# Kernel optimization log

Hardware: AMD Instinct MI355X
Metric: run time of the kernel (lower is better)

The kernel has to match this reference:

```python
import jax, jax.numpy as jnp
import numpy as np

N_BLOCK = 3; EMBED = 256; N_HEAD = 8; HEAD = EMBED // N_HEAD
N_AGENT = 8; SEQ = 256; BATCH = 64; ACT_DIM = 32
DECAY_SCALE = 1.0
EPS = 1e-6


def _decay_matrix():
    # Per-head decay kappas as in Mava Sable, decay over timesteps (pos // n_agent), causal mask.
    gammas = (1.0 - jnp.exp(jnp.linspace(jnp.log(1.0 / 32.0), jnp.log(1.0 / 512.0), N_HEAD))) * DECAY_SCALE
    t = (jnp.arange(SEQ) // N_AGENT).astype(jnp.float32)
    diff = t[:, None] - t[None, :]
    causal = jnp.arange(SEQ)[:, None] >= jnp.arange(SEQ)[None, :]
    return jnp.where(causal[None], gammas[:, None, None] ** diff[None], 0.0)  # [H,S,S]


def rmsnorm(x, scale):
    return x * jax.lax.rsqrt(jnp.mean(x * x, -1, keepdims=True) + EPS) * scale


def groupnorm(x, scale, bias):
    # GroupNorm with n_head groups over the feature dim, per position.
    B, S, E = x.shape
    xg = x.reshape(B, S, N_HEAD, HEAD)
    mu = xg.mean(-1, keepdims=True)
    var = ((xg - mu) ** 2).mean(-1, keepdims=True)
    xn = ((xg - mu) * jax.lax.rsqrt(var + 1e-5)).reshape(B, S, E)
    return xn * scale + bias


def retention(q_in, k_in, v_in, wq, wk, wv, wg, wo, gns, gnb, decay):
    # Parallel multi-scale retention: (Q K^T * D) V, groupnorm, swish gate from query input.
    B, S, E = q_in.shape
    q = (q_in @ wq).reshape(B, S, N_HEAD, HEAD).transpose(0, 2, 1, 3)
    k = (k_in @ wk).reshape(B, S, N_HEAD, HEAD).transpose(0, 2, 1, 3) / jnp.sqrt(jnp.float32(HEAD))
    v = (v_in @ wv).reshape(B, S, N_HEAD, HEAD).transpose(0, 2, 1, 3)
    scores = jnp.einsum('bhnd,bhmd->bhnm', q, k) * decay[None]
    ret = jnp.einsum('bhnm,bhmd->bhnd', scores, v)
    ret = groupnorm(ret.transpose(0, 2, 1, 3).reshape(B, S, E), gns, gnb)
    return (jax.nn.swish(q_in @ wg) * ret) @ wo


def swiglu(x, wg, w1, w2):
    return (jax.nn.swish(x @ wg) * (x @ w1)) @ w2


def forward(action, obs_rep, w_enc, ln0, wq1, wk1, wv1, wg1, wo1, gns1, gnb1, ln1,
            wq2, wk2, wv2, wg2, wo2, gns2, gnb2, ln2, swg, sw1, sw2, ln3,
            hw1, hb1, hln, hw2, hb2):
    decay = _decay_matrix()
    x = rmsnorm(jax.nn.gelu(action @ w_enc), ln0)
    for b in range(N_BLOCK):
        r1 = retention(x, x, x, wq1[b], wk1[b], wv1[b], wg1[b], wo1[b], gns1[b], gnb1[b], decay)
        x = rmsnorm(x + r1, ln1[b])
        r2 = retention(obs_rep, x, x, wq2[b], wk2[b], wv2[b], wg2[b], wo2[b], gns2[b], gnb2[b], decay)
        x = rmsnorm(obs_rep + r2, ln2[b])
        x = rmsnorm(x + swiglu(x, swg[b], sw1[b], sw2[b]), ln3[b])
    h = rmsnorm(jax.nn.gelu(x @ hw1 + hb1), hln)
    return h @ hw2 + hb2


def setup_inputs() -> dict:
    key = jax.random.key(0)
    ks = jax.random.split(key, 24)
    E, A, NB = EMBED, ACT_DIM, N_BLOCK
    s = 0.02
    return {
        'action': jax.random.uniform(ks[0], (BATCH, SEQ, A), jnp.float32),
        'obs_rep': jax.random.normal(ks[1], (BATCH, SEQ, E), jnp.float32),
        'w_enc': jax.random.normal(ks[2], (A, E), jnp.float32) * s,
        'ln0': jnp.ones((E,), jnp.float32),
        'wq1': jax.random.normal(ks[3], (NB, E, E), jnp.float32) * s,
        'wk1': jax.random.normal(ks[4], (NB, E, E), jnp.float32) * s,
        'wv1': jax.random.normal(ks[5], (NB, E, E), jnp.float32) * s,
        'wg1': jax.random.normal(ks[6], (NB, E, E), jnp.float32) * s,
        'wo1': jax.random.normal(ks[7], (NB, E, E), jnp.float32) * s,
        'gns1': jnp.ones((NB, E), jnp.float32),
        'gnb1': jnp.zeros((NB, E), jnp.float32),
        'ln1': jnp.ones((NB, E), jnp.float32),
        'wq2': jax.random.normal(ks[8], (NB, E, E), jnp.float32) * s,
        'wk2': jax.random.normal(ks[9], (NB, E, E), jnp.float32) * s,
        'wv2': jax.random.normal(ks[10], (NB, E, E), jnp.float32) * s,
        'wg2': jax.random.normal(ks[11], (NB, E, E), jnp.float32) * s,
        'wo2': jax.random.normal(ks[12], (NB, E, E), jnp.float32) * s,
        'gns2': jnp.ones((NB, E), jnp.float32),
        'gnb2': jnp.zeros((NB, E), jnp.float32),
        'ln2': jnp.ones((NB, E), jnp.float32),
        'swg': jax.random.normal(ks[13], (NB, E, E), jnp.float32) * s,
        'sw1': jax.random.normal(ks[14], (NB, E, E), jnp.float32) * s,
        'sw2': jax.random.normal(ks[15], (NB, E, E), jnp.float32) * s,
        'ln3': jnp.ones((NB, E), jnp.float32),
        'hw1': jax.random.normal(ks[16], (E, E), jnp.float32) * s,
        'hb1': jnp.zeros((E,), jnp.float32),
        'hln': jnp.ones((E,), jnp.float32),
        'hw2': jax.random.normal(ks[17], (E, A), jnp.float32) * s,
        'hb2': jnp.zeros((A,), jnp.float32),
    }


def reference(action, obs_rep, w_enc, ln0, wq1, wk1, wv1, wg1, wo1, gns1, gnb1, ln1,
              wq2, wk2, wv2, wg2, wo2, gns2, gnb2, ln2, swg, sw1, sw2, ln3,
              hw1, hb1, hln, hw2, hb2):
    return forward(action, obs_rep, w_enc, ln0, wq1, wk1, wv1, wg1, wo1, gns1, gnb1, ln1,
                   wq2, wk2, wv2, wg2, wo2, gns2, gnb2, ln2, swg, sw1, sw2, ln3,
                   hw1, hb1, hln, hw2, hb2)
```

## Files before the change

kernel.cpp:

```cpp
#include <hip/hip_runtime.h>
#include <cstdint>
#include <cmath>

typedef __attribute__((ext_vector_type(8))) short short8;
typedef __attribute__((ext_vector_type(4))) float floatx4;

#define DEV static __device__ __forceinline__

DEV float bf2f(uint16_t u) {
    union { uint32_t i; float f; } v; v.i = ((uint32_t)u) << 16; return v.f;
}
DEV uint16_t f2bf(float f) {
    union { float f; uint32_t i; } v; v.f = f;
    uint32_t r = (v.i + 0x7FFFu + ((v.i >> 16) & 1u)) >> 16;
    return (uint16_t)r;
}
DEV float swishf(float x) { return x / (1.f + __expf(-x)); }
DEV float geluf(float x) {
    const float c = 0.7978845608028654f;
    float t = tanhf(c * (x + 0.044715f * x * x * x));
    return 0.5f * x * (1.f + t);
}

#define CHUNK_E 8192
#define MAT_E   65536
#define APAD    264


struct TArg { const float* src[15]; };

__global__ __launch_bounds__(256) void tpose_k(TArg ta, uint16_t* __restrict__ arena) {
    int z = blockIdx.z;
    const float* src; uint16_t* dst;
    if (z == 0) {
        if (blockIdx.y) return;
        src = ta.src[0]; dst = arena;
    } else if (z <= 39) {
        int q = z - 1; int ti = q / 3, s = q % 3;
        src = ta.src[1 + ti] + (size_t)s * 65536;
        dst = arena + CHUNK_E + (size_t)(ti * 3 + s) * MAT_E;
    } else {
        src = ta.src[14]; dst = arena + CHUNK_E + (size_t)39 * MAT_E;
    }
    int k0 = blockIdx.y << 5;
    int n0 = blockIdx.x << 6;
    __shared__ __align__(16) uint16_t tile[32][72];
    int t = threadIdx.x;
    {
        int r = t >> 3, c = (t & 7) << 3;
        const float* s0 = src + (size_t)(k0 + r) * 256 + n0 + c;
        float4 f0 = *(const float4*)s0;
        float4 f1 = *(const float4*)(s0 + 4);
        tile[r][c + 0] = f2bf(f0.x); tile[r][c + 1] = f2bf(f0.y);
        tile[r][c + 2] = f2bf(f0.z); tile[r][c + 3] = f2bf(f0.w);
        tile[r][c + 4] = f2bf(f1.x); tile[r][c + 5] = f2bf(f1.y);
        tile[r][c + 6] = f2bf(f1.z); tile[r][c + 7] = f2bf(f1.w);
    }
    __syncthreads();
    {
        int n = t >> 2, c = (t & 3) << 3;
        uint16_t tmp[8];
#pragma unroll
        for (int j = 0; j < 8; ++j) tmp[j] = tile[c + j][n];
        *(uint4*)&dst[(size_t)(k0 >> 5) * CHUNK_E + (size_t)(n0 + n) * 32 + c] = *(uint4*)tmp;
    }
}

struct SegArgs {
    const float* action; const float* obs;
    uint16_t *actb, *obsb, *xb, *bq, *bk, *bv, *bg, *brg;
    const float *ln0, *hb1, *hln, *hw2, *hb2;
    float* outp;
    float l2g[8];
};

enum { EP_NONE = 0, EP_GELU_RMS = 1, EP_RESID_RMS = 2 };
enum { EP2_NONE = 0, EP2_SWIGLU = 1 };

template<int EPI, int K, int LDA, bool OG, int LDO, bool RL>
DEV void gemm_u(int m0,
                const uint16_t* __restrict__ A,
                const uint16_t* __restrict__ Wt,
                uint16_t* __restrict__ Og,
                uint16_t* __restrict__ Ol,
                const float* __restrict__ bias,
                const uint16_t* __restrict__ Rg,
                const uint16_t* __restrict__ Rl,
                const float* __restrict__ lnw,
                float (&rowsum)[8][32])
{
    const int t = threadIdx.x;
    const int w = t >> 6, lane = t & 63, l16 = lane & 15, lg = lane >> 4;
    constexpr int NC = K / 32;

    floatx4 acc[2][2];
#pragma unroll
    for (int i = 0; i < 2; ++i)
#pragma unroll
        for (int j = 0; j < 2; ++j) acc[i][j] = (floatx4){0.f, 0.f, 0.f, 0.f};

#pragma unroll
    for (int kc = 0; kc < NC; ++kc) {
        short8 aF[2], bF[2];
#pragma unroll
        for (int rt = 0; rt < 2; ++rt) {
            int row = (rt << 4) + l16;
            if constexpr (LDA != 0)
                aF[rt] = *(const short8*)(A + (size_t)row * LDA + (kc << 5) + (lg << 3));
            else
                aF[rt] = *(const short8*)(A + (size_t)(m0 + row) * K + (kc << 5) + (lg << 3));
        }
#pragma unroll
        for (int ct = 0; ct < 2; ++ct)
            bF[ct] = *(const short8*)(Wt + (size_t)kc * CHUNK_E +
                                      (size_t)((w << 5) + (ct << 4) + l16) * 32 + (lg << 3));
#pragma unroll
        for (int rt = 0; rt < 2; ++rt)
#pragma unroll
            for (int ct = 0; ct < 2; ++ct)
                acc[rt][ct] = __builtin_amdgcn_mfma_f32_16x16x32_bf16(
                    aF[rt], bF[ct], acc[rt][ct], 0, 0, 0);
    }

    float v[2][2][4];
#pragma unroll
    for (int rt = 0; rt < 2; ++rt)
#pragma unroll
        for (int ct = 0; ct < 2; ++ct)
#pragma unroll
            for (int r = 0; r < 4; ++r) {
                int row = (rt << 4) + (lg << 2) + r;
                int col = (w << 5) + (ct << 4) + l16;
                float x = acc[rt][ct][r];
                if constexpr (EPI == EP_GELU_RMS) {
                    if (bias) x += bias[col];
                    x = geluf(x);
                }
                if constexpr (EPI == EP_RESID_RMS) {
                    if constexpr (RL) x += bf2f(Rl[(size_t)row * APAD + col]);
                    else              x += bf2f(Rg[(size_t)(m0 + row) * 256 + col]);
                }
                v[rt][ct][r] = x;
            }

    if constexpr (EPI == EP_GELU_RMS || EPI == EP_RESID_RMS) {
#pragma unroll
        for (int rt = 0; rt < 2; ++rt)
#pragma unroll
            for (int r = 0; r < 4; ++r) {
                float p = v[rt][0][r] * v[rt][0][r] + v[rt][1][r] * v[rt][1][r];
                p += __shfl_xor(p, 1, 64); p += __shfl_xor(p, 2, 64);
                p += __shfl_xor(p, 4, 64); p += __shfl_xor(p, 8, 64);
                int row = (rt << 4) + (lg << 2) + r;
                if (l16 == 0) rowsum[w][row] = p;
            }
        __syncthreads();
#pragma unroll
        for (int rt = 0; rt < 2; ++rt)
#pragma unroll
            for (int r = 0; r < 4; ++r) {
                int row = (rt << 4) + (lg << 2) + r;
                float tot = rowsum[0][row] + rowsum[1][row] + rowsum[2][row] + rowsum[3][row]
                          + rowsum[4][row] + rowsum[5][row] + rowsum[6][row] + rowsum[7][row];
                float rn = rsqrtf(tot * (1.f / 256.f) + 1e-6f);
#pragma unroll
                for (int ct = 0; ct < 2; ++ct) {
                    int col = (w << 5) + (ct << 4) + l16;
                    uint16_t bb = f2bf(v[rt][ct][r] * rn * lnw[col]);
                    if constexpr (OG)
                        Og[(size_t)(m0 + row) * 256 + col] = bb;
                    if constexpr (LDO != 0)
                        Ol[(size_t)row * LDO + col] = bb;
                }
            }
        __syncthreads();
    } else {
#pragma unroll
        for (int rt = 0; rt < 2; ++rt)
#pragma unroll
            for (int ct = 0; ct < 2; ++ct)
#pragma unroll
                for (int r = 0; r < 4; ++r) {
                    int row = (rt << 4) + (lg << 2) + r;
                    int col = (w << 5) + (ct << 4) + l16;
                    uint16_t bb = f2bf(v[rt][ct][r]);
                    if constexpr (OG)
                        Og[(size_t)(m0 + row) * 256 + col] = bb;
                    if constexpr (LDO != 0)
                        Ol[(size_t)row * LDO + col] = bb;
                }
    }
}

template<int EPI, int LDA>
DEV void gemm2_u(int m0, const uint16_t* __restrict__ A,
                 const uint16_t* __restrict__ W1, const uint16_t* __restrict__ W2,
                 uint16_t* __restrict__ O1, uint16_t* __restrict__ O2,
                 uint16_t* __restrict__ Ol)
{
    const int t = threadIdx.x;
    const int w = t >> 6, lane = t & 63, l16 = lane & 15, lg = lane >> 4;

    floatx4 a1[2][2], a2[2][2];
#pragma unroll
    for (int i = 0; i < 2; ++i)
#pragma unroll
        for (int j = 0; j < 2; ++j) {
            a1[i][j] = (floatx4){0.f, 0.f, 0.f, 0.f};
            a2[i][j] = (floatx4){0.f, 0.f, 0.f, 0.f};
        }

#pragma unroll
    for (int kc = 0; kc < 8; ++kc) {
        short8 aF[2], b1[2], b2[2];
#pragma unroll
        for (int rt = 0; rt < 2; ++rt) {
            int row = (rt << 4) + l16;
            if constexpr (LDA != 0)
                aF[rt] = *(const short8*)(A + (size_t)row * LDA + (kc << 5) + (lg << 3));
            else
                aF[rt] = *(const short8*)(A + (size_t)(m0 + row) * 256 + (kc << 5) + (lg << 3));
        }
        size_t woff = (size_t)kc * CHUNK_E + (size_t)((w << 5) + l16) * 32 + (lg << 3);
#pragma unroll
        for (int ct = 0; ct < 2; ++ct) {
            b1[ct] = *(const short8*)(W1 + woff + (size_t)(ct << 4) * 32);
            b2[ct] = *(const short8*)(W2 + woff + (size_t)(ct << 4) * 32);
        }
#pragma unroll
        for (int rt = 0; rt < 2; ++rt)
#pragma unroll
            for (int ct = 0; ct < 2; ++ct) {
                a1[rt][ct] = __builtin_amdgcn_mfma_f32_16x16x32_bf16(aF[rt], b1[ct], a1[rt][ct], 0, 0, 0);
                a2[rt][ct] = __builtin_amdgcn_mfma_f32_16x16x32_bf16(aF[rt], b2[ct], a2[rt][ct], 0, 0, 0);
            }
    }

#pragma unroll
    for (int rt = 0; rt < 2; ++rt)
#pragma unroll
        for (int ct = 0; ct < 2; ++ct)
#pragma unroll
            for (int r = 0; r < 4; ++r) {
                int row = (rt << 4) + (lg << 2) + r;
                int col = (w << 5) + (ct << 4) + l16;
                if constexpr (EPI == EP2_NONE) {
                    size_t idx = (size_t)(m0 + row) * 256 + col;
                    O1[idx] = f2bf(a1[rt][ct][r]);
                    O2[idx] = f2bf(a2[rt][ct][r]);
                } else {
                    Ol[(size_t)row * APAD + col] = f2bf(swishf(a1[rt][ct][r]) * a2[rt][ct][r]);
                }
            }
}

DEV int rowbase(int blk) { return (blk & 63) * 256 + (blk >> 6) * 32; }


__global__ __launch_bounds__(512, 4) void seg0_k(SegArgs sa, const uint16_t* __restrict__ wenc,
                                                 const uint16_t* __restrict__ wq,
                                                 const uint16_t* __restrict__ wk,
                                                 const uint16_t* __restrict__ wv,
                                                 const uint16_t* __restrict__ wg)
{
    __shared__ float rowsum[8][32];
    __shared__ __align__(16) uint16_t actS[32][40];
    __shared__ __align__(16) uint16_t T0[32][APAD];
    const int t = threadIdx.x;
    const int m0 = rowbase(blockIdx.x);
    if (t < 256) {
        int r = t >> 3, c = (t & 7) << 2;
        float4 f = *(const float4*)(sa.action + (size_t)(m0 + r) * 32 + c);
        uint16_t tmp[4] = { f2bf(f.x), f2bf(f.y), f2bf(f.z), f2bf(f.w) };
        *(uint2*)&actS[r][c] = *(uint2*)tmp;
    }
    {
        const float4* ob = (const float4*)sa.obs + (size_t)m0 * 64;
        uint2* od = (uint2*)sa.obsb + (size_t)m0 * 64;
#pragma unroll
        for (int j = 0; j < 4; ++j) {
            float4 f = ob[(j << 9) + t];
            uint16_t tmp[4] = { f2bf(f.x), f2bf(f.y), f2bf(f.z), f2bf(f.w) };
            od[(j << 9) + t] = *(uint2*)tmp;
        }
    }
    __syncthreads();
    gemm_u<EP_GELU_RMS, 32, 40, true, APAD, false>(m0, &actS[0][0], wenc,
        sa.xb, &T0[0][0], nullptr, nullptr, nullptr, sa.ln0, rowsum);
    gemm2_u<EP2_NONE, APAD>(m0, &T0[0][0], wq, wk, sa.bq, sa.bk, nullptr);
    gemm2_u<EP2_NONE, APAD>(m0, &T0[0][0], wv, wg, sa.bv, sa.bg, nullptr);
}

__global__ __launch_bounds__(512, 4) void attn_k(SegArgs sa, const float* __restrict__ gns,
                                                 const float* __restrict__ gnb)
{
    __shared__ __align__(16) uint16_t QS[256][40];
    __shared__ __align__(16) uint16_t Ks[256][40];
    __shared__ __align__(16) uint16_t Vt[32][264];
    const int b = blockIdx.x & 63, h = blockIdx.x >> 6;
    const float l2g = sa.l2g[h];
    const int t = threadIdx.x, w = t >> 6, lane = t & 63, l16 = lane & 15, lg = lane >> 4;
    const size_t base = ((size_t)b * 256) * 256 + (size_t)h * 32;
    const uint16_t *q = sa.bq, *kbuf = sa.bk, *vbuf = sa.bv, *g = sa.bg;
    uint16_t* out = sa.brg;

    if (t < 256) {
        const uint4* qr = (const uint4*)(q + base + (size_t)t * 256);
        *(uint4*)&QS[t][0] = qr[0]; *(uint4*)&QS[t][8] = qr[1];
        *(uint4*)&QS[t][16] = qr[2]; *(uint4*)&QS[t][24] = qr[3];
        const uint4* kr = (const uint4*)(kbuf + base + (size_t)t * 256);
        *(uint4*)&Ks[t][0] = kr[0]; *(uint4*)&Ks[t][8] = kr[1];
        *(uint4*)&Ks[t][16] = kr[2]; *(uint4*)&Ks[t][24] = kr[3];
    } else {
        int c = t - 256;
        union { uint4 v4[4]; uint16_t u[32]; } vv;
        const uint4* vr = (const uint4*)(vbuf + base + (size_t)c * 256);
        vv.v4[0] = vr[0]; vv.v4[1] = vr[1]; vv.v4[2] = vr[2]; vv.v4[3] = vr[3];
#pragma unroll
        for (int d = 0; d < 32; ++d) Vt[d][c] = vv.u[d];
    }
    __syncthreads();

    short8 qF[2];
#pragma unroll
    for (int rt = 0; rt < 2; ++rt)
        qF[rt] = *(const short8*)&QS[(w << 5) + (rt << 4) + l16][lg << 3];

    floatx4 racc[2][2];
#pragma unroll
    for (int i = 0; i < 2; ++i) { racc[i][0] = (floatx4){0,0,0,0}; racc[i][1] = (floatx4){0,0,0,0}; }

    const float invsq = 0.17677669529663687f;
    const int jtmax = w;
    for (int jt = 0; jt <= jtmax; ++jt) {
        const int j0 = jt << 5;
        floatx4 sacc[2][2];
#pragma unroll
        for (int i = 0; i < 2; ++i) { sacc[i][0] = (floatx4){0,0,0,0}; sacc[i][1] = (floatx4){0,0,0,0}; }
        short8 kF[2];
#pragma unroll
        for (int ct = 0; ct < 2; ++ct)
            kF[ct] = *(const short8*)&Ks[j0 + (ct << 4) + l16][lg << 3];
#pragma unroll
        for (int rt = 0; rt < 2; ++rt)
#pragma unroll
            for (int ct = 0; ct < 2; ++ct)
                sacc[rt][ct] = __builtin_amdgcn_mfma_f32_16x16x32_bf16(
                    qF[rt], kF[ct], sacc[rt][ct], 0, 0, 0);
#pragma unroll
        for (int rt = 0; rt < 2; ++rt)
#pragma unroll
            for (int ct = 0; ct < 2; ++ct)
#pragma unroll
                for (int r = 0; r < 4; ++r) {
                    int row = (rt << 4) + (lg << 2) + r;
                    int i = (w << 5) + row;
                    int j = j0 + (ct << 4) + l16;
                    float svv = 0.f;
                    if (i >= j)
                        svv = sacc[rt][ct][r] * invsq *
                              exp2f((float)((i >> 3) - (j >> 3)) * l2g);
                    QS[(w << 5) + row][(ct << 4) + l16] = f2bf(svv);
                }
        short8 vF[2];
#pragma unroll
        for (int ct = 0; ct < 2; ++ct)
            vF[ct] = *(const short8*)&Vt[(ct << 4) + l16][j0 + (lg << 3)];
#pragma unroll
        for (int rt = 0; rt < 2; ++rt) {
            short8 sF = *(const short8*)&QS[(w << 5) + (rt << 4) + l16][lg << 3];
#pragma unroll
            for (int ct = 0; ct < 2; ++ct)
                racc[rt][ct] = __builtin_amdgcn_mfma_f32_16x16x32_bf16(
                    sF, vF[ct], racc[rt][ct], 0, 0, 0);
        }
    }

#pragma unroll
    for (int rt = 0; rt < 2; ++rt)
#pragma unroll
        for (int r = 0; r < 4; ++r) {
            float v0 = racc[rt][0][r], v1 = racc[rt][1][r];
            float s1 = v0 + v1, s2 = v0 * v0 + v1 * v1;
            s1 += __shfl_xor(s1, 1, 64); s2 += __shfl_xor(s2, 1, 64);
            s1 += __shfl_xor(s1, 2, 64); s2 += __shfl_xor(s2, 2, 64);
            s1 += __shfl_xor(s1, 4, 64); s2 += __shfl_xor(s2, 4, 64);
            s1 += __shfl_xor(s1, 8, 64); s2 += __shfl_xor(s2, 8, 64);
            float mu = s1 * (1.f / 32.f);
            float var = s2 * (1.f / 32.f) - mu * mu;
            float rstd = rsqrtf(var + 1e-5f);
            int srow = (w << 5) + (rt << 4) + (lg << 2) + r;
            size_t obase = ((size_t)b * 256 + srow) * 256 + (size_t)h * 32;
#pragma unroll
            for (int ct = 0; ct < 2; ++ct) {
                int d = (ct << 4) + l16;
                float x = ct ? v1 : v0;
                float y = (x - mu) * rstd * gns[h * 32 + d] + gnb[h * 32 + d];
                float gv = swishf(bf2f(g[obase + d]));
                out[obase + d] = f2bf(y * gv);
            }
        }
}

__global__ __launch_bounds__(512, 4) void g1_k(SegArgs sa,
    const uint16_t* __restrict__ wo, const float* __restrict__ ln1,
    const uint16_t* __restrict__ wq, const uint16_t* __restrict__ wk,
    const uint16_t* __restrict__ wv, const uint16_t* __restrict__ wg)
{
    __shared__ float rowsum[8][32];
    __shared__ __align__(16) uint16_t T0[32][APAD];
    const int m0 = rowbase(blockIdx.x);
    gemm_u<EP_RESID_RMS, 256, 0, false, APAD, false>(m0, sa.brg, wo,
        nullptr, &T0[0][0], nullptr, sa.xb, nullptr, ln1, rowsum);
    gemm2_u<EP2_NONE, APAD>(m0, &T0[0][0], wk, wv, sa.bk, sa.bv, nullptr);
    gemm2_u<EP2_NONE, 0>(m0, sa.obsb, wq, wg, sa.bq, sa.bg, nullptr);
}

__global__ __launch_bounds__(512, 4) void g2_k(SegArgs sa,
    const uint16_t* __restrict__ wo, const float* __restrict__ ln2,
    const uint16_t* __restrict__ wswg, const uint16_t* __restrict__ wsw1,
    const uint16_t* __restrict__ wsw2, const float* __restrict__ ln3,
    const uint16_t* __restrict__ nwq, const uint16_t* __restrict__ nwk,
    const uint16_t* __restrict__ nwv, const uint16_t* __restrict__ nwg)
{
    __shared__ float rowsum[8][32];
    __shared__ __align__(16) uint16_t T0[32][APAD];
    __shared__ __align__(16) uint16_t T1[32][APAD];
    const int m0 = rowbase(blockIdx.x);
    gemm_u<EP_RESID_RMS, 256, 0, false, APAD, false>(m0, sa.brg, wo,
        nullptr, &T0[0][0], nullptr, sa.obsb, nullptr, ln2, rowsum);
    gemm2_u<EP2_SWIGLU, APAD>(m0, &T0[0][0], wswg, wsw1, nullptr, nullptr, &T1[0][0]);
    __syncthreads();
    gemm_u<EP_RESID_RMS, 256, APAD, true, APAD, true>(m0, &T1[0][0], wsw2,
        sa.xb, &T0[0][0], nullptr, nullptr, &T0[0][0], ln3, rowsum);
    if (nwq) {
        gemm2_u<EP2_NONE, APAD>(m0, &T0[0][0], nwq, nwk, sa.bq, sa.bk, nullptr);
        gemm2_u<EP2_NONE, APAD>(m0, &T0[0][0], nwv, nwg, sa.bv, sa.bg, nullptr);
    }
}

__global__ __launch_bounds__(512, 4) void head_k(SegArgs sa, const uint16_t* __restrict__ hw1t)
{
    __shared__ float rowsum[8][32];
    __shared__ float w2s[8192];
    __shared__ __align__(16) uint16_t T0[32][APAD];
    const int t = threadIdx.x;
    const int m0 = rowbase(blockIdx.x);
#pragma unroll
    for (int j = 0; j < 16; ++j) w2s[(j << 9) + t] = sa.hw2[(j << 9) + t];
    gemm_u<EP_GELU_RMS, 256, 0, false, APAD, false>(m0, sa.xb, hw1t,
        nullptr, &T0[0][0], sa.hb1, nullptr, nullptr, sa.hln, rowsum);
    {
        int n = t & 31, rs = t >> 5;
#pragma unroll
        for (int rr = 0; rr < 2; ++rr) {
            int lrow = (rr << 4) + rs;
            float a0 = sa.hb2[n];
#pragma unroll 8
            for (int kk = 0; kk < 256; ++kk)
                a0 += bf2f(T0[lrow][kk]) * w2s[kk * 32 + n];
            sa.outp[(size_t)(m0 + lrow) * 32 + n] = a0;
        }
    }
}

extern "C" void kernel_launch(void* const* d_in, const int* in_sizes, int n_in,
                              void* d_out, int out_size, void* d_ws, size_t ws_size,
                              hipStream_t stream)
{
    const float* action = (const float*)d_in[0];
    const float* obs    = (const float*)d_in[1];
    const float* w_enc  = (const float*)d_in[2];
    const float* ln0    = (const float*)d_in[3];
    const float* wq1 = (const float*)d_in[4];
    const float* wk1 = (const float*)d_in[5];
    const float* wv1 = (const float*)d_in[6];
    const float* wg1 = (const float*)d_in[7];
    const float* wo1 = (const float*)d_in[8];
    const float* gns1 = (const float*)d_in[9];
    const float* gnb1 = (const float*)d_in[10];
    const float* ln1  = (const float*)d_in[11];
    const float* wq2 = (const float*)d_in[12];
    const float* wk2 = (const float*)d_in[13];
    const float* wv2 = (const float*)d_in[14];
    const float* wg2 = (const float*)d_in[15];
    const float* wo2 = (const float*)d_in[16];
    const float* gns2 = (const float*)d_in[17];
    const float* gnb2 = (const float*)d_in[18];
    const float* ln2  = (const float*)d_in[19];
    const float* swgp = (const float*)d_in[20];
    const float* sw1p = (const float*)d_in[21];
    const float* sw2p = (const float*)d_in[22];
    const float* ln3  = (const float*)d_in[23];
    const float* hw1  = (const float*)d_in[24];
    const float* hb1  = (const float*)d_in[25];
    const float* hln  = (const float*)d_in[26];
    const float* hw2  = (const float*)d_in[27];
    const float* hb2  = (const float*)d_in[28];

    char* ws = (char*)d_ws;
    uint16_t* wt   = (uint16_t*)(ws + 0);
    uint16_t* actb = (uint16_t*)(ws + 6291456);
    uint16_t* obsb = (uint16_t*)(ws + 7340032);
    uint16_t* xb   = (uint16_t*)(ws + 15728640);
    uint16_t* bq   = (uint16_t*)(ws + 24117248);
    uint16_t* bk   = (uint16_t*)(ws + 32505856);
    uint16_t* bv   = (uint16_t*)(ws + 40894464);
    uint16_t* bg   = (uint16_t*)(ws + 49283072);
    uint16_t* brg  = (uint16_t*)(ws + 57671680);

    uint16_t* wtenc = wt;
    uint16_t* hw1t  = wt + CHUNK_E + (size_t)39 * MAT_E;
    auto WTp = [&](int ti, int s) { return wt + CHUNK_E + (size_t)(ti * 3 + s) * MAT_E; };

    TArg ta;
    ta.src[0] = w_enc;
    ta.src[1] = wq1;  ta.src[2] = wk1;  ta.src[3] = wv1;  ta.src[4] = wg1;  ta.src[5] = wo1;
    ta.src[6] = wq2;  ta.src[7] = wk2;  ta.src[8] = wv2;  ta.src[9] = wg2;  ta.src[10] = wo2;
    ta.src[11] = swgp; ta.src[12] = sw1p; ta.src[13] = sw2p; ta.src[14] = hw1;
    tpose_k<<<dim3(4, 8, 41), 256, 0, stream>>>(ta, wt);

    SegArgs sa;
    sa.action = action; sa.obs = obs;
    sa.actb = actb; sa.obsb = obsb; sa.xb = xb;
    sa.bq = bq; sa.bk = bk; sa.bv = bv; sa.bg = bg; sa.brg = brg;
    sa.ln0 = ln0; sa.hb1 = hb1; sa.hln = hln; sa.hw2 = hw2; sa.hb2 = hb2;
    sa.outp = (float*)d_out;
    {
        const double a = log(1.0 / 32.0), bb = log(1.0 / 512.0);
        for (int hh = 0; hh < 8; ++hh) {
            double lg = a + (bb - a) * hh / 7.0;
            double gam = 1.0 - exp(lg);
            sa.l2g[hh] = (float)(log(gam) / log(2.0));
        }
    }

    dim3 GB(512), TB(512);
    seg0_k<<<GB, TB, 0, stream>>>(sa, wtenc, WTp(0, 0), WTp(1, 0), WTp(2, 0), WTp(3, 0));
    for (int b3 = 0; b3 < 3; ++b3) {
        attn_k<<<GB, TB, 0, stream>>>(sa, gns1 + b3 * 256, gnb1 + b3 * 256);
        g1_k<<<GB, TB, 0, stream>>>(sa, WTp(4, b3), ln1 + b3 * 256,
                                    WTp(5, b3), WTp(6, b3), WTp(7, b3), WTp(8, b3));
        attn_k<<<GB, TB, 0, stream>>>(sa, gns2 + b3 * 256, gnb2 + b3 * 256);
        g2_k<<<GB, TB, 0, stream>>>(sa, WTp(9, b3), ln2 + b3 * 256,
                                    WTp(10, b3), WTp(11, b3), WTp(12, b3), ln3 + b3 * 256,
                                    b3 < 2 ? WTp(0, b3 + 1) : nullptr,
                                    b3 < 2 ? WTp(1, b3 + 1) : nullptr,
                                    b3 < 2 ? WTp(2, b3 + 1) : nullptr,
                                    b3 < 2 ? WTp(3, b3 + 1) : nullptr);
    }
    head_k<<<GB, TB, 0, stream>>>(sa, hw1t);
}
```

Baseline: 555.1 us.

## Halve GEMM row tiles to double grid size and balance causal attention strips

GEMM-style kernels now process 16 rows per block instead of 32, doubling the grid to 1024 blocks and raising the launch-bounds occupancy hint. The attention kernel assigns each wave two 16-row query strips (w and 15-w) so the causal triangle work is balanced across waves instead of wave 7 doing eight times the work of wave 0. The aim is better CU utilization and less tail imbalance, at the cost of reloading each weight tile for half as many rows per block.

Measured after the change: 689.9 us. +24.3%, slower.

```diff
diff --git a/kernel.cpp b/kernel.cpp
--- a/kernel.cpp
+++ b/kernel.cpp
@@ -77,7 +77,7 @@
 enum { EP_NONE = 0, EP_GELU_RMS = 1, EP_RESID_RMS = 2 };
 enum { EP2_NONE = 0, EP2_SWIGLU = 1 };
 
-template<int EPI, int K, int LDA, bool OG, int LDO, bool RL>
+template<int EPI, int K, int LDA, bool OG, int LDO, bool RL, int ROWS>
 DEV void gemm_u(int m0,
                 const uint16_t* __restrict__ A,
                 const uint16_t* __restrict__ Wt,
@@ -87,23 +87,24 @@
                 const uint16_t* __restrict__ Rg,
                 const uint16_t* __restrict__ Rl,
                 const float* __restrict__ lnw,
-                float (&rowsum)[8][32])
+                float (&rowsum)[8][ROWS])
 {
     const int t = threadIdx.x;
     const int w = t >> 6, lane = t & 63, l16 = lane & 15, lg = lane >> 4;
     constexpr int NC = K / 32;
-
-    floatx4 acc[2][2];
-#pragma unroll
-    for (int i = 0; i < 2; ++i)
+    constexpr int RT = ROWS / 16;
+
+    floatx4 acc[RT][2];
+#pragma unroll
+    for (int i = 0; i < RT; ++i)
 #pragma unroll
         for (int j = 0; j < 2; ++j) acc[i][j] = (floatx4){0.f, 0.f, 0.f, 0.f};
 
 #pragma unroll
     for (int kc = 0; kc < NC; ++kc) {
-        short8 aF[2], bF[2];
-#pragma unroll
-        for (int rt = 0; rt < 2; ++rt) {
+        short8 aF[RT], bF[2];
+#pragma unroll
+        for (int rt = 0; rt < RT; ++rt) {
             int row = (rt << 4) + l16;
             if constexpr (LDA != 0)
                 aF[rt] = *(const short8*)(A + (size_t)row * LDA + (kc << 5) + (lg << 3));
@@ -115,16 +116,16 @@
             bF[ct] = *(const short8*)(Wt + (size_t)kc * CHUNK_E +
                                       (size_t)((w << 5) + (ct << 4) + l16) * 32 + (lg << 3));
 #pragma unroll
-        for (int rt = 0; rt < 2; ++rt)
+        for (int rt = 0; rt < RT; ++rt)
 #pragma unroll
             for (int ct = 0; ct < 2; ++ct)
                 acc[rt][ct] = __builtin_amdgcn_mfma_f32_16x16x32_bf16(
                     aF[rt], bF[ct], acc[rt][ct], 0, 0, 0);
     }
 
-    float v[2][2][4];
-#pragma unroll
-    for (int rt = 0; rt < 2; ++rt)
+    float v[RT][2][4];
+#pragma unroll
+    for (int rt = 0; rt < RT; ++rt)
 #pragma unroll
         for (int ct = 0; ct < 2; ++ct)
 #pragma unroll
@@ -145,7 +146,7 @@
 
     if constexpr (EPI == EP_GELU_RMS || EPI == EP_RESID_RMS) {
 #pragma unroll
-        for (int rt = 0; rt < 2; ++rt)
+        for (int rt = 0; rt < RT; ++rt)
 #pragma unroll
             for (int r = 0; r < 4; ++r) {
                 float p = v[rt][0][r] * v[rt][0][r] + v[rt][1][r] * v[rt][1][r];
@@ -156,7 +157,7 @@
             }
         __syncthreads();
 #pragma unroll
-        for (int rt = 0; rt < 2; ++rt)
+        for (int rt = 0; rt < RT; ++rt)
 #pragma unroll
             for (int r = 0; r < 4; ++r) {
                 int row = (rt << 4) + (lg << 2) + r;
@@ -176,7 +177,7 @@
         __syncthreads();
     } else {
 #pragma unroll
-        for (int rt = 0; rt < 2; ++rt)
+        for (int rt = 0; rt < RT; ++rt)
 #pragma unroll
             for (int ct = 0; ct < 2; ++ct)
 #pragma unroll
@@ -192,7 +193,7 @@
     }
 }
 
-template<int EPI, int LDA>
+template<int EPI, int LDA, int ROWS>
 DEV void gemm2_u(int m0, const uint16_t* __restrict__ A,
                  const uint16_t* __restrict__ W1, const uint16_t* __restrict__ W2,
                  uint16_t* __restrict__ O1, uint16_t* __restrict__ O2,
@@ -200,10 +201,11 @@
 {
     const int t = threadIdx.x;
     const int w = t >> 6, lane = t & 63, l16 = lane & 15, lg = lane >> 4;
-
-    floatx4 a1[2][2], a2[2][2];
-#pragma unroll
-    for (int i = 0; i < 2; ++i)
+    constexpr int RT = ROWS / 16;
+
+    floatx4 a1[RT][2], a2[RT][2];
+#pragma unroll
+    for (int i = 0; i < RT; ++i)
 #pragma unroll
         for (int j = 0; j < 2; ++j) {
             a1[i][j] = (floatx4){0.f, 0.f, 0.f, 0.f};
@@ -212,9 +214,9 @@
 
 #pragma unroll
     for (int kc = 0; kc < 8; ++kc) {
-        short8 aF[2], b1[2], b2[2];
-#pragma unroll
-        for (int rt = 0; rt < 2; ++rt) {
+        short8 aF[RT], b1[2], b2[2];
+#pragma unroll
+        for (int rt = 0; rt < RT; ++rt) {
             int row = (rt << 4) + l16;
             if constexpr (LDA != 0)
                 aF[rt] = *(const short8*)(A + (size_t)row * LDA + (kc << 5) + (lg << 3));
@@ -228,7 +230,7 @@
             b2[ct] = *(const short8*)(W2 + woff + (size_t)(ct << 4) * 32);
         }
 #pragma unroll
-        for (int rt = 0; rt < 2; ++rt)
+        for (int rt = 0; rt < RT; ++rt)
 #pragma unroll
             for (int ct = 0; ct < 2; ++ct) {
                 a1[rt][ct] = __builtin_amdgcn_mfma_f32_16x16x32_bf16(aF[rt], b1[ct], a1[rt][ct], 0, 0, 0);
@@ -237,7 +239,7 @@
     }
 
 #pragma unroll
-    for (int rt = 0; rt < 2; ++rt)
+    for (int rt = 0; rt < RT; ++rt)
 #pragma unroll
         for (int ct = 0; ct < 2; ++ct)
 #pragma unroll
@@ -254,21 +256,21 @@
             }
 }
 
-DEV int rowbase(int blk) { return (blk & 63) * 256 + (blk >> 6) * 32; }
-
-
-__global__ __launch_bounds__(512, 4) void seg0_k(SegArgs sa, const uint16_t* __restrict__ wenc,
+DEV int rowbase16(int blk) { return (blk & 63) * 256 + (blk >> 6) * 16; }
+
+
+__global__ __launch_bounds__(512, 8) void seg0_k(SegArgs sa, const uint16_t* __restrict__ wenc,
                                                  const uint16_t* __restrict__ wq,
                                                  const uint16_t* __restrict__ wk,
                                                  const uint16_t* __restrict__ wv,
                                                  const uint16_t* __restrict__ wg)
 {
-    __shared__ float rowsum[8][32];
-    __shared__ __align__(16) uint16_t actS[32][40];
-    __shared__ __align__(16) uint16_t T0[32][APAD];
+    __shared__ float rowsum[8][16];
+    __shared__ __align__(16) uint16_t actS[16][40];
+    __shared__ __align__(16) uint16_t T0[16][APAD];
     const int t = threadIdx.x;
-    const int m0 = rowbase(blockIdx.x);
-    if (t < 256) {
+    const int m0 = rowbase16(blockIdx.x);
+    if (t < 128) {
         int r = t >> 3, c = (t & 7) << 2;
         float4 f = *(const float4*)(sa.action + (size_t)(m0 + r) * 32 + c);
         uint16_t tmp[4] = { f2bf(f.x), f2bf(f.y), f2bf(f.z), f2bf(f.w) };
@@ -278,17 +280,17 @@
         const float4* ob = (const float4*)sa.obs + (size_t)m0 * 64;
         uint2* od = (uint2*)sa.obsb + (size_t)m0 * 64;
 #pragma unroll
-        for (int j = 0; j < 4; ++j) {
+        for (int j = 0; j < 2; ++j) {
             float4 f = ob[(j << 9) + t];
             uint16_t tmp[4] = { f2bf(f.x), f2bf(f.y), f2bf(f.z), f2bf(f.w) };
             od[(j << 9) + t] = *(uint2*)tmp;
         }
     }
     __syncthreads();
-    gemm_u<EP_GELU_RMS, 32, 40, true, APAD, false>(m0, &actS[0][0], wenc,
+    gemm_u<EP_GELU_RMS, 32, 40, true, APAD, false, 16>(m0, &actS[0][0], wenc,
         sa.xb, &T0[0][0], nullptr, nullptr, nullptr, sa.ln0, rowsum);
-    gemm2_u<EP2_NONE, APAD>(m0, &T0[0][0], wq, wk, sa.bq, sa.bk, nullptr);
-    gemm2_u<EP2_NONE, APAD>(m0, &T0[0][0], wv, wg, sa.bv, sa.bg, nullptr);
+    gemm2_u<EP2_NONE, APAD, 16>(m0, &T0[0][0], wq, wk, sa.bq, sa.bk, nullptr);
+    gemm2_u<EP2_NONE, APAD, 16>(m0, &T0[0][0], wv, wg, sa.bv, sa.bg, nullptr);
 }
 
 __global__ __launch_bounds__(512, 4) void attn_k(SegArgs sa, const float* __restrict__ gns,
@@ -321,66 +323,61 @@
     }
     __syncthreads();
 
-    short8 qF[2];
-#pragma unroll
-    for (int rt = 0; rt < 2; ++rt)
-        qF[rt] = *(const short8*)&QS[(w << 5) + (rt << 4) + l16][lg << 3];
-
-    floatx4 racc[2][2];
-#pragma unroll
-    for (int i = 0; i < 2; ++i) { racc[i][0] = (floatx4){0,0,0,0}; racc[i][1] = (floatx4){0,0,0,0}; }
+    const int iA = w, iB = 15 - w;
+    short8 qFA = *(const short8*)&QS[(iA << 4) + l16][lg << 3];
+    short8 qFB = *(const short8*)&QS[(iB << 4) + l16][lg << 3];
 
     const float invsq = 0.17677669529663687f;
-    const int jtmax = w;
-    for (int jt = 0; jt <= jtmax; ++jt) {
-        const int j0 = jt << 5;
-        floatx4 sacc[2][2];
-#pragma unroll
-        for (int i = 0; i < 2; ++i) { sacc[i][0] = (floatx4){0,0,0,0}; sacc[i][1] = (floatx4){0,0,0,0}; }
-        short8 kF[2];
-#pragma unroll
-        for (int ct = 0; ct < 2; ++ct)
-            kF[ct] = *(const short8*)&Ks[j0 + (ct << 4) + l16][lg << 3];
-#pragma unroll
-        for (int rt = 0; rt < 2; ++rt)
-#pragma unroll
-            for (int ct = 0; ct < 2; ++ct)
-                sacc[rt][ct] = __builtin_amdgcn_mfma_f32_16x16x32_bf16(
-                    qF[rt], kF[ct], sacc[rt][ct], 0, 0, 0);
-#pragma unroll
-        for (int rt = 0; rt < 2; ++rt)
+
+    floatx4 raccA[2], raccB[2];
+    raccA[0] = (floatx4){0,0,0,0}; raccA[1] = (floatx4){0,0,0,0};
+    raccB[0] = (floatx4){0,0,0,0}; raccB[1] = (floatx4){0,0,0,0};
+
+    auto do_strip = [&](int si, short8 qF, floatx4 (&racc)[2]) {
+        const int jtmax = ((si << 4) + 15) >> 5;
+        for (int jt = 0; jt <= jtmax; ++jt) {
+            const int j0 = jt << 5;
+            floatx4 sacc[2];
+            sacc[0] = (floatx4){0,0,0,0}; sacc[1] = (floatx4){0,0,0,0};
+            short8 kF[2];
+#pragma unroll
+            for (int ct = 0; ct < 2; ++ct)
+                kF[ct] = *(const short8*)&Ks[j0 + (ct << 4) + l16][lg << 3];
+#pragma unroll
+            for (int ct = 0; ct < 2; ++ct)
+                sacc[ct] = __builtin_amdgcn_mfma_f32_16x16x32_bf16(
+                    qF, kF[ct], sacc[ct], 0, 0, 0);
 #pragma unroll
             for (int ct = 0; ct < 2; ++ct)
 #pragma unroll
                 for (int r = 0; r < 4; ++r) {
-                    int row = (rt << 4) + (lg << 2) + r;
-                    int i = (w << 5) + row;
+                    int row16 = (lg << 2) + r;
+                    int i = (si << 4) + row16;
                     int j = j0 + (ct << 4) + l16;
                     float svv = 0.f;
                     if (i >= j)
-                        svv = sacc[rt][ct][r] * invsq *
+                        svv = sacc[ct][r] * invsq *
                               exp2f((float)((i >> 3) - (j >> 3)) * l2g);
-                    QS[(w << 5) + row][(ct << 4) + l16] = f2bf(svv);
+                    QS[(si << 4) + row16][(ct << 4) + l16] = f2bf(svv);
                 }
-        short8 vF[2];
-#pragma unroll
-        for (int ct = 0; ct < 2; ++ct)
-            vF[ct] = *(const short8*)&Vt[(ct << 4) + l16][j0 + (lg << 3)];
-#pragma unroll
-        for (int rt = 0; rt < 2; ++rt) {
-            short8 sF = *(const short8*)&QS[(w << 5) + (rt << 4) + l16][lg << 3];
-#pragma unroll
-            for (int ct = 0; ct < 2; ++ct)
-                racc[rt][ct] = __builtin_amdgcn_mfma_f32_16x16x32_bf16(
-                    sF, vF[ct], racc[rt][ct], 0, 0, 0);
-        }
-    }
-
-#pragma unroll
-    for (int rt = 0; rt < 2; ++rt)
+            short8 vF[2];
+#pragma unroll
+            for (int ct = 0; ct < 2; ++ct)
+                vF[ct] = *(const short8*)&Vt[(ct << 4) + l16][j0 + (lg << 3)];
+            short8 sF = *(const short8*)&QS[(si << 4) + l16][lg << 3];
+#pragma unroll
+            for (int ct = 0; ct < 2; ++ct)
+                racc[ct] = __builtin_amdgcn_mfma_f32_16x16x32_bf16(
+                    sF, vF[ct], racc[ct], 0, 0, 0);
+        }
+    };
+    do_strip(iA, qFA, raccA);
+    do_strip(iB, qFB, raccB);
+
+    auto epi = [&](int si, floatx4 (&racc)[2]) {
 #pragma unroll
         for (int r = 0; r < 4; ++r) {
-            float v0 = racc[rt][0][r], v1 = racc[rt][1][r];
+            float v0 = racc[0][r], v1 = racc[1][r];
             float s1 = v0 + v1, s2 = v0 * v0 + v1 * v1;
             s1 += __shfl_xor(s1, 1, 64); s2 += __shfl_xor(s2, 1, 64);
             s1 += __shfl_xor(s1, 2, 64); s2 += __shfl_xor(s2, 2, 64);
@@ -389,7 +386,7 @@
             float mu = s1 * (1.f / 32.f);
             float var = s2 * (1.f / 32.f) - mu * mu;
             float rstd = rsqrtf(var + 1e-5f);
-            int srow = (w << 5) + (rt << 4) + (lg << 2) + r;
+            int srow = (si << 4) + (lg << 2) + r;
             size_t obase = ((size_t)b * 256 + srow) * 256 + (size_t)h * 32;
 #pragma unroll
             for (int ct = 0; ct < 2; ++ct) {
@@ -400,67 +397,66 @@
                 out[obase + d] = f2bf(y * gv);
             }
         }
-}
-
-__global__ __launch_bounds__(512, 4) void g1_k(SegArgs sa,
+    };
+    epi(iA, raccA);
+    epi(iB, raccB);
+}
+
+__global__ __launch_bounds__(512, 8) void g1_k(SegArgs sa,
     const uint16_t* __restrict__ wo, const float* __restrict__ ln1,
     const uint16_t* __restrict__ wq, const uint16_t* __restrict__ wk,
     const uint16_t* __restrict__ wv, const uint16_t* __restrict__ wg)
 {
-    __shared__ float rowsum[8][32];
-    __shared__ __align__(16) uint16_t T0[32][APAD];
-    const int m0 = rowbase(blockIdx.x);
-    gemm_u<EP_RESID_RMS, 256, 0, false, APAD, false>(m0, sa.brg, wo,
+    __shared__ float rowsum[8][16];
+    __shared__ __align__(16) uint16_t T0[16][APAD];
+    const int m0 = rowbase16(blockIdx.x);
+    gemm_u<EP_RESID_RMS, 256, 0, false, APAD, false, 16>(m0, sa.brg, wo,
         nullptr, &T0[0][0], nullptr, sa.xb, nullptr, ln1, rowsum);
-    gemm2_u<EP2_NONE, APAD>(m0, &T0[0][0], wk, wv, sa.bk, sa.bv, nullptr);
-    gemm2_u<EP2_NONE, 0>(m0, sa.obsb, wq, wg, sa.bq, sa.bg, nullptr);
-}
-
-__global__ __launch_bounds__(512, 4) void g2_k(SegArgs sa,
+    gemm2_u<EP2_NONE, APAD, 16>(m0, &T0[0][0], wk, wv, sa.bk, sa.bv, nullptr);
+    gemm2_u<EP2_NONE, 0, 16>(m0, sa.obsb, wq, wg, sa.bq, sa.bg, nullptr);
+}
+
+__global__ __launch_bounds__(512, 8) void g2_k(SegArgs sa,
     const uint16_t* __restrict__ wo, const float* __restrict__ ln2,
     const uint16_t* __restrict__ wswg, const uint16_t* __restrict__ wsw1,
     const uint16_t* __restrict__ wsw2, const float* __restrict__ ln3,
     const uint16_t* __restrict__ nwq, const uint16_t* __restrict__ nwk,
     const uint16_t* __restrict__ nwv, const uint16_t* __restrict__ nwg)
 {
-    __shared__ float rowsum[8][32];
-    __shared__ __align__(16) uint16_t T0[32][APAD];
-    __shared__ __align__(16) uint16_t T1[32][APAD];
-    const int m0 = rowbase(blockIdx.x);
-    gemm_u<EP_RESID_RMS, 256, 0, false, APAD, false>(m0, sa.brg, wo,
+    __shared__ float rowsum[8][16];
+    __shared__ __align__(16) uint16_t T0[16][APAD];
+    __shared__ __align__(16) uint16_t T1[16][APAD];
+    const int m0 = rowbase16(blockIdx.x);
+    gemm_u<EP_RESID_RMS, 256, 0, false, APAD, false, 16>(m0, sa.brg, wo,
         nullptr, &T0[0][0], nullptr, sa.obsb, nullptr, ln2, rowsum);
-    gemm2_u<EP2_SWIGLU, APAD>(m0, &T0[0][0], wswg, wsw1, nullptr, nullptr, &T1[0][0]);
+    gemm2_u<EP2_SWIGLU, APAD, 16>(m0, &T0[0][0], wswg, wsw1, nullptr, nullptr, &T1[0][0]);
     __syncthreads();
-    gemm_u<EP_RESID_RMS, 256, APAD, true, APAD, true>(m0, &T1[0][0], wsw2,
+    gemm_u<EP_RESID_RMS, 256, APAD, true, APAD, true, 16>(m0, &T1[0][0], wsw2,
         sa.xb, &T0[0][0], nullptr, nullptr, &T0[0][0], ln3, rowsum);
     if (nwq) {
-        gemm2_u<EP2_NONE, APAD>(m0, &T0[0][0], nwq, nwk, sa.bq, sa.bk, nullptr);
-        gemm2_u<EP2_NONE, APAD>(m0, &T0[0][0], nwv, nwg, sa.bv, sa.bg, nullptr);
-    }
-}
-
-__global__ __launch_bounds__(512, 4) void head_k(SegArgs sa, const uint16_t* __restrict__ hw1t)
-{
-    __shared__ float rowsum[8][32];
+        gemm2_u<EP2_NONE, APAD, 16>(m0, &T0[0][0], nwq, nwk, sa.bq, sa.bk, nullptr);
+        gemm2_u<EP2_NONE, APAD, 16>(m0, &T0[0][0], nwv, nwg, sa.bv, sa.bg, nullptr);
+    }
+}
+
+__global__ __launch_bounds__(512, 8) void head_k(SegArgs sa, const uint16_t* __restrict__ hw1t)
+{
+    __shared__ float rowsum[8][16];
     __shared__ float w2s[8192];
-    __shared__ __align__(16) uint16_t T0[32][APAD];
+    __shared__ __align__(16) uint16_t T0[16][APAD];
     const int t = threadIdx.x;
-    const int m0 = rowbase(blockIdx.x);
+    const int m0 = rowbase16(blockIdx.x);
 #pragma unroll
     for (int j = 0; j < 16; ++j) w2s[(j << 9) + t] = sa.hw2[(j << 9) + t];
-    gemm_u<EP_GELU_RMS, 256, 0, false, APAD, false>(m0, sa.xb, hw1t,
+    gemm_u<EP_GELU_RMS, 256, 0, false, APAD, false, 16>(m0, sa.xb, hw1t,
         nullptr, &T0[0][0], sa.hb1, nullptr, nullptr, sa.hln, rowsum);
     {
         int n = t & 31, rs = t >> 5;
-#pragma unroll
-        for (int rr = 0; rr < 2; ++rr) {
-            int lrow = (rr << 4) + rs;
-            float a0 = sa.hb2[n];
+        float a0 = sa.hb2[n];
 #pragma unroll 8
-            for (int kk = 0; kk < 256; ++kk)
-                a0 += bf2f(T0[lrow][kk]) * w2s[kk * 32 + n];
-            sa.outp[(size_t)(m0 + lrow) * 32 + n] = a0;
-        }
+        for (int kk = 0; kk < 256; ++kk)
+            a0 += bf2f(T0[rs][kk]) * w2s[kk * 32 + n];
+        sa.outp[(size_t)(m0 + rs) * 32 + n] = a0;
     }
 }
 
@@ -535,19 +531,19 @@
         }
     }
 
-    dim3 GB(512), TB(512);
-    seg0_k<<<GB, TB, 0, stream>>>(sa, wtenc, WTp(0, 0), WTp(1, 0), WTp(2, 0), WTp(3, 0));
+    dim3 GBg(1024), GBa(512), TB(512);
+    seg0_k<<<GBg, TB, 0, stream>>>(sa, wtenc, WTp(0, 0), WTp(1, 0), WTp(2, 0), WTp(3, 0));
     for (int b3 = 0; b3 < 3; ++b3) {
-        attn_k<<<GB, TB, 0, stream>>>(sa, gns1 + b3 * 256, gnb1 + b3 * 256);
-        g1_k<<<GB, TB, 0, stream>>>(sa, WTp(4, b3), ln1 + b3 * 256,
-                                    WTp(5, b3), WTp(6, b3), WTp(7, b3), WTp(8, b3));
-        attn_k<<<GB, TB, 0, stream>>>(sa, gns2 + b3 * 256, gnb2 + b3 * 256);
-        g2_k<<<GB, TB, 0, stream>>>(sa, WTp(9, b3), ln2 + b3 * 256,
-                                    WTp(10, b3), WTp(11, b3), WTp(12, b3), ln3 + b3 * 256,
-                                    b3 < 2 ? WTp(0, b3 + 1) : nullptr,
-                                    b3 < 2 ? WTp(1, b3 + 1) : nullptr,
-                                    b3 < 2 ? WTp(2, b3 + 1) : nullptr,
-                                    b3 < 2 ? WTp(3, b3 + 1) : nullptr);
-    }
-    head_k<<<GB, TB, 0, stream>>>(sa, hw1t);
-}
+        attn_k<<<GBa, TB, 0, stream>>>(sa, gns1 + b3 * 256, gnb1 + b3 * 256);
+        g1_k<<<GBg, TB, 0, stream>>>(sa, WTp(4, b3), ln1 + b3 * 256,
+                                     WTp(5, b3), WTp(6, b3), WTp(7, b3), WTp(8, b3));
+        attn_k<<<GBa, TB, 0, stream>>>(sa, gns2 + b3 * 256, gnb2 + b3 * 256);
+        g2_k<<<GBg, TB, 0, stream>>>(sa, WTp(9, b3), ln2 + b3 * 256,
+                                     WTp(10, b3), WTp(11, b3), WTp(12, b3), ln3 + b3 * 256,
+                                     b3 < 2 ? WTp(0, b3 + 1) : nullptr,
+                                     b3 < 2 ? WTp(1, b3 + 1) : nullptr,
+                                     b3 < 2 ? WTp(2, b3 + 1) : nullptr,
+                                     b3 < 2 ? WTp(3, b3 + 1) : nullptr);
+    }
+    head_k<<<GBg, TB, 0, stream>>>(sa, hw1t);
+}
```
